# Optimization experiments

Hardware: AMD Instinct MI355X
Metric: run time of the kernel (lower is better)

## Reference

```python
import jax, jax.numpy as jnp
import numpy as np
import math

S = 8192
D = 128

def setup_inputs() -> dict:
    key = jax.random.key(0)
    kq, kk, kv = jax.random.split(key, 3)
    q = jax.random.normal(kq, (S, D), dtype=jnp.float32)
    k = jax.random.normal(kk, (S, D), dtype=jnp.float32)
    v = jax.random.normal(kv, (S, D), dtype=jnp.float32)
    return {"q": q, "k": k, "v": v}

def reference(q, k, v):
    # scores: [Sq, Sk], scaled by sqrt(head_dim)
    scale = 1.0 / math.sqrt(q.shape[1])
    scores = jnp.einsum('qd,kd->qk', q, k) * scale
    # causal mask: tril kept, strict upper triangle -> -inf (mask=True)
    causal = jnp.tril(jnp.ones((q.shape[0], k.shape[0]), dtype=bool))
    scores = jnp.where(causal, scores, -jnp.inf)
    # softmax over keys (dim=1), numerically stable
    attn = jax.nn.softmax(scores, axis=1)
    return jnp.einsum('qk,kd->qd', attn, v)
```

## Files before the change

kernel.cpp:

```cpp
#include <hip/hip_runtime.h>

#define S_TOTAL 8192
#define D_DIM   128
#define QBLK    256
#define NQT     32
#define NSPL    16
#define UNITS   512
#define TILEB   16384
#define QSCALE  0.12751879523178264f
#define NEG_BIG -1.0e30f
#define THR     8.0f

typedef __attribute__((ext_vector_type(8)))  short    bf16x8;
typedef __attribute__((ext_vector_type(16))) float    f32x16;
typedef __attribute__((ext_vector_type(4)))  float    f32x4;
typedef __attribute__((ext_vector_type(4)))  unsigned u32x4;

static __device__ __forceinline__ unsigned short f2bf(float f) {
    unsigned int u = __builtin_bit_cast(unsigned int, f);
    u += 0x7FFFu + ((u >> 16) & 1u);
    return (unsigned short)(u >> 16);
}
static __device__ __forceinline__ float bf2f(unsigned short u) {
    return __builtin_bit_cast(float, (unsigned int)u << 16);
}
static __device__ __forceinline__ void glds16(const void* g, void* l) {
    __builtin_amdgcn_global_load_lds(
        (const __attribute__((address_space(1))) void*)g,
        (__attribute__((address_space(3))) void*)l, 16, 0, 0);
}
static __device__ __forceinline__ unsigned pk2(float lo, float hi) {
    unsigned r;
    asm("v_cvt_pk_bf16_f32 %0, %1, %2" : "=v"(r) : "v"(lo), "v"(hi));
    return r;
}
static __device__ __forceinline__ void pl32swap(unsigned& x, unsigned& y) {
    asm("v_permlane32_swap_b32 %0, %1" : "+v"(x), "+v"(y));
}

__global__ __launch_bounds__(256)
void prep_q(const float* __restrict__ Q, unsigned short* __restrict__ Qbf)
{
    int i4 = blockIdx.x * 256 + threadIdx.x;
    const float4 v = reinterpret_cast<const float4*>(Q)[i4];
    ushort4 o;
    o.x = f2bf(v.x * QSCALE); o.y = f2bf(v.y * QSCALE);
    o.z = f2bf(v.z * QSCALE); o.w = f2bf(v.w * QSCALE);
    reinterpret_cast<ushort4*>(Qbf)[i4] = o;
}

__global__ __launch_bounds__(256)
void prep_k(const float* __restrict__ K, unsigned short* __restrict__ Kswz)
{
    int c = blockIdx.x * 256 + threadIdx.x;
    int t = c >> 10;
    int r = (c >> 4) & 63;
    int slot = c & 15;
    int d0 = (slot ^ (r & 15)) << 3;
    const float* src = K + ((size_t)t * 64 + r) * D_DIM + d0;
    float4 a = *reinterpret_cast<const float4*>(src);
    float4 b = *reinterpret_cast<const float4*>(src + 4);
    bf16x8 o;
    o[0] = (short)f2bf(a.x); o[1] = (short)f2bf(a.y);
    o[2] = (short)f2bf(a.z); o[3] = (short)f2bf(a.w);
    o[4] = (short)f2bf(b.x); o[5] = (short)f2bf(b.y);
    o[6] = (short)f2bf(b.z); o[7] = (short)f2bf(b.w);
    *reinterpret_cast<bf16x8*>(&Kswz[(size_t)c * 8]) = o;
}

__global__ __launch_bounds__(256)
void prep_v(const float* __restrict__ V, unsigned short* __restrict__ Vt)
{
    __shared__ float sv[64 * 68];
    int t = blockIdx.x >> 1;
    int h = blockIdx.x & 1;
    #pragma unroll
    for (int it = 0; it < 4; ++it) {
        int f4 = it * 256 + threadIdx.x;
        int r   = f4 >> 4;
        int c16 = (f4 & 15) << 2;
        float4 v = *reinterpret_cast<const float4*>(
            V + ((size_t)t * 64 + r) * D_DIM + h * 64 + c16);
        sv[r * 68 + c16 + 0] = v.x;
        sv[r * 68 + c16 + 1] = v.y;
        sv[r * 68 + c16 + 2] = v.z;
        sv[r * 68 + c16 + 3] = v.w;
    }
    __syncthreads();
    #pragma unroll
    for (int ii = 0; ii < 2; ++ii) {
        int cl = threadIdx.x * 2 + ii;
        int dl = cl >> 3;
        int slot = cl & 7;
        int d = h * 64 + dl;
        int k0 = (slot ^ (d & 7)) << 3;
        bf16x8 o;
        #pragma unroll
        for (int i = 0; i < 8; ++i) o[i] = (short)f2bf(sv[(k0 + i) * 68 + dl]);
        *reinterpret_cast<bf16x8*>(&Vt[(size_t)t * 8192 + ((size_t)(d * 8 + slot)) * 8]) = o;
    }
}

#define PROC_SUB(QF, ACC, MR, LR, QSB)                                        \
  {                                                                           \
    const int qg_ = (QSB) + qc;                                               \
    f32x16 sc;                                                                \
    _Pragma("unroll")                                                         \
    for (int r = 0; r < 16; ++r) sc[r] = 0.0f;                                \
    {                                                                         \
      const int rK_ = kj * 32 + qc;                                           \
      __builtin_amdgcn_s_setprio(1);                                          \
      _Pragma("unroll")                                                       \
      for (int dc = 0; dc < 8; ++dc) {                                        \
        int slot_ = ((dc << 1) | hi) ^ (rK_ & 15);                            \
        bf16x8 kf_ = *reinterpret_cast<const bf16x8*>(                        \
            bK + (rK_ << 8) + (slot_ << 4));                                  \
        sc = __builtin_amdgcn_mfma_f32_32x32x16_bf16(kf_, QF[dc], sc, 0, 0, 0); \
      }                                                                       \
      __builtin_amdgcn_s_setprio(0);                                          \
    }                                                                         \
    if (kbase + 31 > (QSB)) {                                                 \
      _Pragma("unroll")                                                       \
      for (int r = 0; r < 16; ++r) {                                          \
        int kg_ = kbase + (r & 3) + 8 * (r >> 2) + 4 * hi;                    \
        if (kg_ > qg_) sc[r] = -INFINITY;                                     \
      }                                                                       \
    }                                                                         \
    float ma_ = fmaxf(fmaxf(sc[0],  sc[1]),  fmaxf(sc[2],  sc[3]));           \
    float mb_ = fmaxf(fmaxf(sc[4],  sc[5]),  fmaxf(sc[6],  sc[7]));           \
    float mc_ = fmaxf(fmaxf(sc[8],  sc[9]),  fmaxf(sc[10], sc[11]));          \
    float md_ = fmaxf(fmaxf(sc[12], sc[13]), fmaxf(sc[14], sc[15]));          \
    float mx_ = fmaxf(fmaxf(ma_, mb_), fmaxf(mc_, md_));                      \
    float tmax_ = fmaxf(mx_, __shfl_xor(mx_, 32));                            \
    if (__any(tmax_ > MR + THR)) {                                            \
      float mn_ = fmaxf(MR, tmax_);                                           \
      float fs_ = __builtin_amdgcn_exp2f(MR - mn_);                           \
      MR = mn_;                                                               \
      LR *= fs_;                                                              \
      _Pragma("unroll")                                                       \
      for (int dt = 0; dt < 4; ++dt)                                          \
        _Pragma("unroll")                                                     \
        for (int r = 0; r < 16; ++r) ACC[dt][r] *= fs_;                       \
    }                                                                         \
    float s0_ = 0.f, s1_ = 0.f, s2_ = 0.f, s3_ = 0.f;                         \
    _Pragma("unroll")                                                         \
    for (int r = 0; r < 16; r += 4) {                                         \
      float p0_ = __builtin_amdgcn_exp2f(sc[r + 0] - MR);                     \
      float p1_ = __builtin_amdgcn_exp2f(sc[r + 1] - MR);                     \
      float p2_ = __builtin_amdgcn_exp2f(sc[r + 2] - MR);                     \
      float p3_ = __builtin_amdgcn_exp2f(sc[r + 3] - MR);                     \
      sc[r + 0] = p0_; sc[r + 1] = p1_; sc[r + 2] = p2_; sc[r + 3] = p3_;     \
      s0_ += p0_; s1_ += p1_; s2_ += p2_; s3_ += p3_;                         \
    }                                                                         \
    float lt_ = (s0_ + s1_) + (s2_ + s3_);                                    \
    lt_ += __shfl_xor(lt_, 32);                                               \
    LR += lt_;                                                                \
    _Pragma("unroll")                                                         \
    for (int cl = 0; cl < 2; ++cl) {                                          \
      const int rb_ = cl * 8;                                                 \
      const int ck_ = kj * 2 + cl;                                            \
      unsigned pa_ = pk2(sc[rb_ + 0], sc[rb_ + 1]);                           \
      unsigned pb_ = pk2(sc[rb_ + 4], sc[rb_ + 5]);                           \
      unsigned pc_ = pk2(sc[rb_ + 2], sc[rb_ + 3]);                           \
      unsigned pd_ = pk2(sc[rb_ + 6], sc[rb_ + 7]);                           \
      pl32swap(pa_, pb_);                                                     \
      pl32swap(pc_, pd_);                                                     \
      u32x4 t4_ = {pa_, pc_, pb_, pd_};                                       \
      bf16x8 pf_ = __builtin_bit_cast(bf16x8, t4_);                           \
      __builtin_amdgcn_s_setprio(1);                                          \
      _Pragma("unroll")                                                       \
      for (int dt = 0; dt < 4; ++dt) {                                        \
        int dV_ = dt * 32 + qc;                                               \
        int slot_ = ((ck_ << 1) | hi) ^ (dV_ & 7);                            \
        bf16x8 vf_ = *reinterpret_cast<const bf16x8*>(                        \
            bV + (dV_ << 7) + (slot_ << 4));                                  \
        ACC[dt] = __builtin_amdgcn_mfma_f32_32x32x16_bf16(vf_, pf_, ACC[dt], 0, 0, 0); \
      }                                                                       \
      __builtin_amdgcn_s_setprio(0);                                          \
    }                                                                         \
  }

#define EPI_SUB(ACC, ROFF, MR, LR)                                            \
  {                                                                           \
    _Pragma("unroll")                                                         \
    for (int dt = 0; dt < 4; ++dt)                                            \
      _Pragma("unroll")                                                       \
      for (int i = 0; i < 8; ++i) {                                           \
        unsigned pk_ = pk2(ACC[dt][2 * i], ACC[dt][2 * i + 1]);               \
        int d_ = dt * 32 + (i & 1) * 2 + (i >> 1) * 8 + 4 * hi;               \
        *reinterpret_cast<unsigned*>(&sOw[qc * 136 + d_]) = pk_;              \
      }                                                                       \
    _Pragma("unroll")                                                         \
    for (int it = 0; it < 8; ++it) {                                          \
      int flat_ = it * 64 + lane;                                             \
      int q_  = flat_ >> 4;                                                   \
      int s8_ = flat_ & 15;                                                   \
      bf16x8 v_ = *reinterpret_cast<const bf16x8*>(&sOw[q_ * 136 + s8_ * 8]); \
      __builtin_nontemporal_store(v_, reinterpret_cast<bf16x8*>(              \
          OB + ((size_t)(w * 64 + (ROFF) + q_)) * D_DIM + s8_ * 8));          \
    }                                                                         \
    if (hi == 0) {                                                            \
      mpart[unit * QBLK + w * 64 + (ROFF) + qc] = MR;                         \
      lpart[unit * QBLK + w * 64 + (ROFF) + qc] = LR;                         \
    }                                                                         \
  }

__global__ __launch_bounds__(256, 2)
void attn16(const unsigned short* __restrict__ Qbf,
            const unsigned short* __restrict__ Kswz,
            const unsigned short* __restrict__ Vtswz,
            unsigned short* __restrict__ Opart,
            float* __restrict__ mpart, float* __restrict__ lpart)
{
    __shared__ char sbuf[2][2 * TILEB];

    const int bx = (int)blockIdx.x;
    const int p  = bx >> 4;
    const int s  = bx & 15;
    const int qt = (p < 16) ? (31 - p) : (p - 16);
    const int unit   = qt * NSPL + s;
    const int jtiles = 4 * qt + 4;

    const int tid  = threadIdx.x;
    const int w    = tid >> 6;
    const int lane = tid & 63;
    const int qc   = lane & 31;
    const int hi   = lane >> 5;

    const int qw0 = qt * QBLK + w * 64;

    bf16x8 qf0[8], qf1[8];
    #pragma unroll
    for (int dc = 0; dc < 8; ++dc) {
        qf0[dc] = *reinterpret_cast<const bf16x8*>(
            Qbf + (size_t)(qw0 + qc) * D_DIM + dc * 16 + hi * 8);
        qf1[dc] = *reinterpret_cast<const bf16x8*>(
            Qbf + (size_t)(qw0 + 32 + qc) * D_DIM + dc * 16 + hi * 8);
    }

    f32x16 acc0[4], acc1[4];
    #pragma unroll
    for (int dt = 0; dt < 4; ++dt)
        #pragma unroll
        for (int r = 0; r < 16; ++r) { acc0[dt][r] = 0.0f; acc1[dt][r] = 0.0f; }
    float m0r = NEG_BIG, l0r = 0.0f, m1r = NEG_BIG, l1r = 0.0f;

    auto STAGE = [&](int c, int j) {
        const char* gK = (const char*)Kswz + (size_t)j * TILEB;
        const char* gV = (const char*)Vtswz + (size_t)j * TILEB;
        char* lK = sbuf[c];
        char* lV = sbuf[c] + TILEB;
        #pragma unroll
        for (int it = 0; it < 4; ++it) {
            int goff = (it * 256 + tid) * 16;
            int loff = (it * 256 + (w << 6)) * 16;
            glds16(gK + goff, lK + loff);
            glds16(gV + goff, lV + loff);
        }
    };

    int j = s, c = 0;
    if (j < jtiles) {
        STAGE(0, j);
        __syncthreads();
        for (; j < jtiles; j += NSPL) {
            int jn = j + NSPL;
            if (jn < jtiles) STAGE(c ^ 1, jn);

            const char* bK = sbuf[c];
            const char* bV = sbuf[c] + TILEB;

            #pragma unroll
            for (int kj = 0; kj < 2; ++kj) {
                const int kbase = j * 64 + kj * 32;
                if (kbase <= qw0 + 63) {
                    if (kbase <= qw0 + 31)
                        PROC_SUB(qf0, acc0, m0r, l0r, qw0);
                    PROC_SUB(qf1, acc1, m1r, l1r, qw0 + 32);
                }
            }
            __syncthreads();
            c ^= 1;
        }
    }

    unsigned short* OB = Opart + (size_t)unit * (QBLK * D_DIM);
    unsigned short* sOw = reinterpret_cast<unsigned short*>(&sbuf[0][0])
                          + w * (32 * 136 + 16);
    EPI_SUB(acc0, 0,  m0r, l0r);
    EPI_SUB(acc1, 32, m1r, l1r);
}

__global__ __launch_bounds__(256)
void attn_mergeF(const unsigned short* __restrict__ Opart,
                 const float* __restrict__ mpart, const float* __restrict__ lpart,
                 float* __restrict__ Og)
{
    int tid = threadIdx.x;
    int row = blockIdx.x * 16 + (tid >> 4);
    int c8  = tid & 15;
    int qt    = row >> 8;
    int local = row & 255;
    int base  = qt * NSPL;

    float M = NEG_BIG;
    for (int s = 0; s < NSPL; ++s)
        M = fmaxf(M, mpart[(size_t)(base + s) * QBLK + local]);
    float L = 0.0f;
    for (int s = 0; s < NSPL; ++s)
        L += __builtin_amdgcn_exp2f(mpart[(size_t)(base + s) * QBLK + local] - M)
             * lpart[(size_t)(base + s) * QBLK + local];
    float invL = 1.0f / L;

    float a[8] = {0.f, 0.f, 0.f, 0.f, 0.f, 0.f, 0.f, 0.f};
    for (int s = 0; s < NSPL; ++s) {
        float e = __builtin_amdgcn_exp2f(mpart[(size_t)(base + s) * QBLK + local] - M);
        bf16x8 o = __builtin_nontemporal_load(reinterpret_cast<const bf16x8*>(
            &Opart[((size_t)(base + s) * QBLK + local) * D_DIM + c8 * 8]));
        #pragma unroll
        for (int i = 0; i < 8; ++i)
            a[i] += e * bf2f((unsigned short)o[i]);
    }
    float4 w0 = {a[0] * invL, a[1] * invL, a[2] * invL, a[3] * invL};
    float4 w1 = {a[4] * invL, a[5] * invL, a[6] * invL, a[7] * invL};
    float* dst = Og + (size_t)row * D_DIM + c8 * 8;
    *reinterpret_cast<float4*>(dst)     = w0;
    *reinterpret_cast<float4*>(dst + 4) = w1;
}

__global__ __launch_bounds__(256, 2)
void attn_f32(const float* __restrict__ Qg, const float* __restrict__ Kg,
              const float* __restrict__ Vg, float* __restrict__ Og)
{
    __shared__ unsigned short sK [64 * 128];
    __shared__ unsigned short sVt[128 * 64];
    __shared__ unsigned short sP [4 * 16 * 72];

    const int qt   = (int)gridDim.y - 1 - (int)blockIdx.y;
    const int tid  = threadIdx.x;
    const int w    = tid >> 6;
    const int lane = tid & 63;
    const int g    = lane >> 4;
    const int lr   = lane & 15;

    const int qrow_base  = qt * 64 + w * 16 + g * 4;
    const int q_frag_row = qt * 64 + w * 16 + lr;

    bf16x8 qa[4];
    #pragma unroll
    for (int dc = 0; dc < 4; ++dc) {
        const float* src = Qg + q_frag_row * D_DIM + dc * 32 + g * 8;
        bf16x8 v;
        #pragma unroll
        for (int i = 0; i < 8; ++i) v[i] = (short)f2bf(src[i]);
        qa[dc] = v;
    }

    f32x4 acc[8];
    #pragma unroll
    for (int dj = 0; dj < 8; ++dj) acc[dj] = f32x4{0.f, 0.f, 0.f, 0.f};
    float m_run[4], l_run[4];
    #pragma unroll
    for (int r = 0; r < 4; ++r) { m_run[r] = -INFINITY; l_run[r] = 0.0f; }

    const float scale = 0.08838834764831845f;
    const int jtiles = qt + 1;
    unsigned short* sPw = sP + w * (16 * 72);
    char* sKc = reinterpret_cast<char*>(sK);
    char* sVc = reinterpret_cast<char*>(sVt);

    for (int j = 0; j < jtiles; ++j) {
        __syncthreads();
        #pragma unroll
        for (int it = 0; it < 8; ++it) {
            int flat4 = it * 256 + tid;
            int r  = flat4 >> 5;
            int d0 = (flat4 & 31) << 2;
            const float4 kv = *reinterpret_cast<const float4*>(
                Kg + (j * 64 + r) * D_DIM + d0);
            ushort4 wv;
            wv.x = f2bf(kv.x); wv.y = f2bf(kv.y); wv.z = f2bf(kv.z); wv.w = f2bf(kv.w);
            int byte = (r << 8) | (((d0 >> 3) ^ (r & 15)) << 4) | ((d0 & 7) << 1);
            *reinterpret_cast<ushort4*>(sKc + byte) = wv;
        }
        {
            int d = tid & 127;
            int khalf = tid >> 7;
            #pragma unroll
            for (int it = 0; it < 8; ++it) {
                int k0 = it * 8 + khalf * 4;
                const float* vsrc = Vg + (j * 64 + k0) * D_DIM + d;
                ushort4 wv;
                wv.x = f2bf(vsrc[0 * D_DIM]); wv.y = f2bf(vsrc[1 * D_DIM]);
                wv.z = f2bf(vsrc[2 * D_DIM]); wv.w = f2bf(vsrc[3 * D_DIM]);
                int byte = (d << 7) | (((k0 >> 3) ^ (d & 7)) << 4) | ((k0 & 7) << 1);
                *reinterpret_cast<ushort4*>(sVc + byte) = wv;
            }
        }
        __syncthreads();

        f32x4 sf[4];
        #pragma unroll
        for (int kj = 0; kj < 4; ++kj) {
            f32x4 accs = f32x4{0.f, 0.f, 0.f, 0.f};
            #pragma unroll
            for (int dc = 0; dc < 4; ++dc) {
                int rowk = kj * 16 + lr;
                int slot = (dc * 4 + g) ^ lr;
                bf16x8 b = *reinterpret_cast<bf16x8*>(sKc + ((rowk << 8) | (slot << 4)));
                accs = __builtin_amdgcn_mfma_f32_16x16x32_bf16(qa[dc], b, accs, 0, 0, 0);
            }
            sf[kj] = accs;
        }
        #pragma unroll
        for (int kj = 0; kj < 4; ++kj)
            #pragma unroll
            for (int r = 0; r < 4; ++r)
                sf[kj][r] *= scale;
        if (j == qt) {
            #pragma unroll
            for (int kj = 0; kj < 4; ++kj) {
                int kglob = j * 64 + kj * 16 + lr;
                #pragma unroll
                for (int r = 0; r < 4; ++r)
                    if (kglob > qrow_base + r) sf[kj][r] = -INFINITY;
            }
        }
        float tmax[4];
        #pragma unroll
        for (int r = 0; r < 4; ++r)
            tmax[r] = fmaxf(fmaxf(sf[0][r], sf[1][r]), fmaxf(sf[2][r], sf[3][r]));
        #pragma unroll
        for (int off = 1; off < 16; off <<= 1)
            #pragma unroll
            for (int r = 0; r < 4; ++r)
                tmax[r] = fmaxf(tmax[r], __shfl_xor(tmax[r], off));
        float fsc[4], lt[4];
        #pragma unroll
        for (int r = 0; r < 4; ++r) {
            float mn = fmaxf(m_run[r], tmax[r]);
            fsc[r] = __expf(m_run[r] - mn);
            m_run[r] = mn;
            lt[r] = 0.0f;
        }
        #pragma unroll
        for (int kj = 0; kj < 4; ++kj)
            #pragma unroll
            for (int r = 0; r < 4; ++r) {
                float p = __expf(sf[kj][r] - m_run[r]);
                sf[kj][r] = p;
                lt[r] += p;
            }
        #pragma unroll
        for (int off = 1; off < 16; off <<= 1)
            #pragma unroll
            for (int r = 0; r < 4; ++r)
                lt[r] += __shfl_xor(lt[r], off);
        #pragma unroll
        for (int r = 0; r < 4; ++r)
            l_run[r] = l_run[r] * fsc[r] + lt[r];
        #pragma unroll
        for (int dj = 0; dj < 8; ++dj)
            #pragma unroll
            for (int r = 0; r < 4; ++r)
                acc[dj][r] *= fsc[r];
        #pragma unroll
        for (int kj = 0; kj < 4; ++kj)
            #pragma unroll
            for (int r = 0; r < 4; ++r)
                sPw[(g * 4 + r) * 72 + kj * 16 + lr] = f2bf(sf[kj][r]);
        bf16x8 pa[2];
        #pragma unroll
        for (int kc = 0; kc < 2; ++kc)
            pa[kc] = *reinterpret_cast<bf16x8*>(sPw + lr * 72 + kc * 32 + g * 8);
        #pragma unroll
        for (int dj = 0; dj < 8; ++dj) {
            #pragma unroll
            for (int kc = 0; kc < 2; ++kc) {
                int d = dj * 16 + lr;
                int slot = (kc * 4 + g) ^ (lr & 7);
                bf16x8 b = *reinterpret_cast<bf16x8*>(sVc + ((d << 7) | (slot << 4)));
                acc[dj] = __builtin_amdgcn_mfma_f32_16x16x32_bf16(pa[kc], b, acc[dj], 0, 0, 0);
            }
        }
    }
    #pragma unroll
    for (int r = 0; r < 4; ++r) {
        float inv = 1.0f / l_run[r];
        int row = qrow_base + r;
        #pragma unroll
        for (int dj = 0; dj < 8; ++dj)
            Og[row * D_DIM + dj * 16 + lr] = acc[dj][r] * inv;
    }
}

extern "C" void kernel_launch(void* const* d_in, const int* in_sizes, int n_in,
                              void* d_out, int out_size, void* d_ws, size_t ws_size,
                              hipStream_t stream)
{
    const float* Qg = (const float*)d_in[0];
    const float* Kg = (const float*)d_in[1];
    const float* Vg = (const float*)d_in[2];
    float* Og = (float*)d_out;

    const size_t bfElems = (size_t)S_TOTAL * D_DIM;
    const size_t need = 3 * bfElems * 2
                      + (size_t)UNITS * ((size_t)QBLK * D_DIM * 2
                                         + (size_t)QBLK * 8);

    if (d_ws == nullptr || ws_size < need) {
        hipLaunchKernelGGL(attn_f32, dim3(1, 128), dim3(256), 0, stream,
                           Qg, Kg, Vg, Og);
        return;
    }

    unsigned short* Qbf   = (unsigned short*)d_ws;
    unsigned short* Kswz  = Qbf + bfElems;
    unsigned short* Vt    = Kswz + bfElems;
    unsigned short* Opart = Vt + bfElems;
    float* mpart = (float*)(Opart + (size_t)UNITS * QBLK * D_DIM);
    float* lpart = mpart + (size_t)UNITS * QBLK;

    hipLaunchKernelGGL(prep_q, dim3(1024), dim3(256), 0, stream, Qg, Qbf);
    hipLaunchKernelGGL(prep_k, dim3(512),  dim3(256), 0, stream, Kg, Kswz);
    hipLaunchKernelGGL(prep_v, dim3(256),  dim3(256), 0, stream, Vg, Vt);

    hipLaunchKernelGGL(attn16, dim3(UNITS), dim3(256), 0, stream,
                       Qbf, Kswz, Vt, Opart, mpart, lpart);
    hipLaunchKernelGGL(attn_mergeF, dim3(S_TOTAL / 16), dim3(256), 0, stream,
                       Opart, mpart, lpart, Og);
}
```

Baseline: 69.03 us.

## Fuse Q conversion into attention, merge K/V prep, interleave two sub-tiles

Drops the separate prep_q kernel and instead loads fp32 Q in the attention kernel, converting and scaling it in registers. prep_k and prep_v are merged into one launch selected by block index, cutting kernel launches from five to three. The per-subtile processing is split into QK^T, softmax and PV macros, and the two query sub-tiles are interleaved so one sub-tile's MFMA work can overlap the other's softmax. The causal mask is now applied unconditionally and the qf0 sub-tile skip for fully masked key blocks is removed, which adds redundant work on diagonal tiles and raises register pressure.

After: 84.13 us. 1.22x slower.

```diff
diff --git a/kernel.cpp b/kernel.cpp
--- a/kernel.cpp
+++ b/kernel.cpp
@@ -39,97 +39,83 @@
 }
 
 __global__ __launch_bounds__(256)
-void prep_q(const float* __restrict__ Q, unsigned short* __restrict__ Qbf)
-{
-    int i4 = blockIdx.x * 256 + threadIdx.x;
-    const float4 v = reinterpret_cast<const float4*>(Q)[i4];
-    ushort4 o;
-    o.x = f2bf(v.x * QSCALE); o.y = f2bf(v.y * QSCALE);
-    o.z = f2bf(v.z * QSCALE); o.w = f2bf(v.w * QSCALE);
-    reinterpret_cast<ushort4*>(Qbf)[i4] = o;
-}
-
-__global__ __launch_bounds__(256)
-void prep_k(const float* __restrict__ K, unsigned short* __restrict__ Kswz)
-{
-    int c = blockIdx.x * 256 + threadIdx.x;
-    int t = c >> 10;
-    int r = (c >> 4) & 63;
-    int slot = c & 15;
-    int d0 = (slot ^ (r & 15)) << 3;
-    const float* src = K + ((size_t)t * 64 + r) * D_DIM + d0;
-    float4 a = *reinterpret_cast<const float4*>(src);
-    float4 b = *reinterpret_cast<const float4*>(src + 4);
-    bf16x8 o;
-    o[0] = (short)f2bf(a.x); o[1] = (short)f2bf(a.y);
-    o[2] = (short)f2bf(a.z); o[3] = (short)f2bf(a.w);
-    o[4] = (short)f2bf(b.x); o[5] = (short)f2bf(b.y);
-    o[6] = (short)f2bf(b.z); o[7] = (short)f2bf(b.w);
-    *reinterpret_cast<bf16x8*>(&Kswz[(size_t)c * 8]) = o;
-}
-
-__global__ __launch_bounds__(256)
-void prep_v(const float* __restrict__ V, unsigned short* __restrict__ Vt)
+void prep_kv(const float* __restrict__ K, const float* __restrict__ V,
+             unsigned short* __restrict__ Kswz, unsigned short* __restrict__ Vt)
 {
     __shared__ float sv[64 * 68];
-    int t = blockIdx.x >> 1;
-    int h = blockIdx.x & 1;
-    #pragma unroll
-    for (int it = 0; it < 4; ++it) {
-        int f4 = it * 256 + threadIdx.x;
-        int r   = f4 >> 4;
-        int c16 = (f4 & 15) << 2;
-        float4 v = *reinterpret_cast<const float4*>(
-            V + ((size_t)t * 64 + r) * D_DIM + h * 64 + c16);
-        sv[r * 68 + c16 + 0] = v.x;
-        sv[r * 68 + c16 + 1] = v.y;
-        sv[r * 68 + c16 + 2] = v.z;
-        sv[r * 68 + c16 + 3] = v.w;
-    }
-    __syncthreads();
-    #pragma unroll
-    for (int ii = 0; ii < 2; ++ii) {
-        int cl = threadIdx.x * 2 + ii;
-        int dl = cl >> 3;
-        int slot = cl & 7;
-        int d = h * 64 + dl;
-        int k0 = (slot ^ (d & 7)) << 3;
+    const int b   = (int)blockIdx.x;
+    const int tid = threadIdx.x;
+
+    if (b < 512) {
+        int c = b * 256 + tid;
+        int t = c >> 10;
+        int r = (c >> 4) & 63;
+        int slot = c & 15;
+        int d0 = (slot ^ (r & 15)) << 3;
+        const float* src = K + ((size_t)t * 64 + r) * D_DIM + d0;
+        float4 a  = *reinterpret_cast<const float4*>(src);
+        float4 bq = *reinterpret_cast<const float4*>(src + 4);
         bf16x8 o;
-        #pragma unroll
-        for (int i = 0; i < 8; ++i) o[i] = (short)f2bf(sv[(k0 + i) * 68 + dl]);
-        *reinterpret_cast<bf16x8*>(&Vt[(size_t)t * 8192 + ((size_t)(d * 8 + slot)) * 8]) = o;
-    }
-}
-
-#define PROC_SUB(QF, ACC, MR, LR, QSB)                                        \
-  {                                                                           \
-    const int qg_ = (QSB) + qc;                                               \
-    f32x16 sc;                                                                \
+        o[0] = (short)f2bf(a.x);  o[1] = (short)f2bf(a.y);
+        o[2] = (short)f2bf(a.z);  o[3] = (short)f2bf(a.w);
+        o[4] = (short)f2bf(bq.x); o[5] = (short)f2bf(bq.y);
+        o[6] = (short)f2bf(bq.z); o[7] = (short)f2bf(bq.w);
+        *reinterpret_cast<bf16x8*>(&Kswz[(size_t)c * 8]) = o;
+    } else {
+        int bb = b - 512;
+        int t = bb >> 1;
+        int h = bb & 1;
+        #pragma unroll
+        for (int it = 0; it < 4; ++it) {
+            int f4 = it * 256 + tid;
+            int r   = f4 >> 4;
+            int c16 = (f4 & 15) << 2;
+            float4 v = *reinterpret_cast<const float4*>(
+                V + ((size_t)t * 64 + r) * D_DIM + h * 64 + c16);
+            sv[r * 68 + c16 + 0] = v.x;
+            sv[r * 68 + c16 + 1] = v.y;
+            sv[r * 68 + c16 + 2] = v.z;
+            sv[r * 68 + c16 + 3] = v.w;
+        }
+        __syncthreads();
+        #pragma unroll
+        for (int ii = 0; ii < 2; ++ii) {
+            int cl = tid * 2 + ii;
+            int dl = cl >> 3;
+            int slot = cl & 7;
+            int d = h * 64 + dl;
+            int k0 = (slot ^ (d & 7)) << 3;
+            bf16x8 o;
+            #pragma unroll
+            for (int i = 0; i < 8; ++i) o[i] = (short)f2bf(sv[(k0 + i) * 68 + dl]);
+            *reinterpret_cast<bf16x8*>(&Vt[(size_t)t * 8192 + ((size_t)(d * 8 + slot)) * 8]) = o;
+        }
+    }
+}
+
+#define QKT_M(SC, QF)                                                         \
+  { _Pragma("unroll")                                                         \
+    for (int r = 0; r < 16; ++r) SC[r] = 0.0f;                                \
+    __builtin_amdgcn_s_setprio(1);                                            \
     _Pragma("unroll")                                                         \
-    for (int r = 0; r < 16; ++r) sc[r] = 0.0f;                                \
-    {                                                                         \
-      const int rK_ = kj * 32 + qc;                                           \
-      __builtin_amdgcn_s_setprio(1);                                          \
-      _Pragma("unroll")                                                       \
-      for (int dc = 0; dc < 8; ++dc) {                                        \
-        int slot_ = ((dc << 1) | hi) ^ (rK_ & 15);                            \
-        bf16x8 kf_ = *reinterpret_cast<const bf16x8*>(                        \
-            bK + (rK_ << 8) + (slot_ << 4));                                  \
-        sc = __builtin_amdgcn_mfma_f32_32x32x16_bf16(kf_, QF[dc], sc, 0, 0, 0); \
-      }                                                                       \
-      __builtin_amdgcn_s_setprio(0);                                          \
+    for (int dc = 0; dc < 8; ++dc) {                                          \
+      bf16x8 kf_ = *reinterpret_cast<const bf16x8*>(                          \
+          bK + (rK << 8) + ((((dc << 1) | hi) ^ (rK & 15)) << 4));            \
+      SC = __builtin_amdgcn_mfma_f32_32x32x16_bf16(kf_, QF[dc], SC, 0, 0, 0); \
     }                                                                         \
-    if (kbase + 31 > (QSB)) {                                                 \
-      _Pragma("unroll")                                                       \
-      for (int r = 0; r < 16; ++r) {                                          \
-        int kg_ = kbase + (r & 3) + 8 * (r >> 2) + 4 * hi;                    \
-        if (kg_ > qg_) sc[r] = -INFINITY;                                     \
-      }                                                                       \
+    __builtin_amdgcn_s_setprio(0); }
+
+#define SM_M(SC, MR, LR, ACC, QSB)                                            \
+  { const int qg_ = (QSB) + qc;                                               \
+    _Pragma("unroll")                                                         \
+    for (int r = 0; r < 16; ++r) {                                            \
+      int kg_ = kbase + (r & 3) + 8 * (r >> 2) + 4 * hi;                      \
+      SC[r] = (kg_ > qg_) ? -INFINITY : SC[r];                                \
     }                                                                         \
-    float ma_ = fmaxf(fmaxf(sc[0],  sc[1]),  fmaxf(sc[2],  sc[3]));           \
-    float mb_ = fmaxf(fmaxf(sc[4],  sc[5]),  fmaxf(sc[6],  sc[7]));           \
-    float mc_ = fmaxf(fmaxf(sc[8],  sc[9]),  fmaxf(sc[10], sc[11]));          \
-    float md_ = fmaxf(fmaxf(sc[12], sc[13]), fmaxf(sc[14], sc[15]));          \
+    float ma_ = fmaxf(fmaxf(SC[0],  SC[1]),  fmaxf(SC[2],  SC[3]));           \
+    float mb_ = fmaxf(fmaxf(SC[4],  SC[5]),  fmaxf(SC[6],  SC[7]));           \
+    float mc_ = fmaxf(fmaxf(SC[8],  SC[9]),  fmaxf(SC[10], SC[11]));          \
+    float md_ = fmaxf(fmaxf(SC[12], SC[13]), fmaxf(SC[14], SC[15]));          \
     float mx_ = fmaxf(fmaxf(ma_, mb_), fmaxf(mc_, md_));                      \
     float tmax_ = fmaxf(mx_, __shfl_xor(mx_, 32));                            \
     if (__any(tmax_ > MR + THR)) {                                            \
@@ -145,24 +131,26 @@
     float s0_ = 0.f, s1_ = 0.f, s2_ = 0.f, s3_ = 0.f;                         \
     _Pragma("unroll")                                                         \
     for (int r = 0; r < 16; r += 4) {                                         \
-      float p0_ = __builtin_amdgcn_exp2f(sc[r + 0] - MR);                     \
-      float p1_ = __builtin_amdgcn_exp2f(sc[r + 1] - MR);                     \
-      float p2_ = __builtin_amdgcn_exp2f(sc[r + 2] - MR);                     \
-      float p3_ = __builtin_amdgcn_exp2f(sc[r + 3] - MR);                     \
-      sc[r + 0] = p0_; sc[r + 1] = p1_; sc[r + 2] = p2_; sc[r + 3] = p3_;     \
+      float p0_ = __builtin_amdgcn_exp2f(SC[r + 0] - MR);                     \
+      float p1_ = __builtin_amdgcn_exp2f(SC[r + 1] - MR);                     \
+      float p2_ = __builtin_amdgcn_exp2f(SC[r + 2] - MR);                     \
+      float p3_ = __builtin_amdgcn_exp2f(SC[r + 3] - MR);                     \
+      SC[r + 0] = p0_; SC[r + 1] = p1_; SC[r + 2] = p2_; SC[r + 3] = p3_;     \
       s0_ += p0_; s1_ += p1_; s2_ += p2_; s3_ += p3_;                         \
     }                                                                         \
     float lt_ = (s0_ + s1_) + (s2_ + s3_);                                    \
     lt_ += __shfl_xor(lt_, 32);                                               \
-    LR += lt_;                                                                \
-    _Pragma("unroll")                                                         \
+    LR += lt_; }
+
+#define PV_M(SC, ACC)                                                         \
+  { _Pragma("unroll")                                                         \
     for (int cl = 0; cl < 2; ++cl) {                                          \
       const int rb_ = cl * 8;                                                 \
       const int ck_ = kj * 2 + cl;                                            \
-      unsigned pa_ = pk2(sc[rb_ + 0], sc[rb_ + 1]);                           \
-      unsigned pb_ = pk2(sc[rb_ + 4], sc[rb_ + 5]);                           \
-      unsigned pc_ = pk2(sc[rb_ + 2], sc[rb_ + 3]);                           \
-      unsigned pd_ = pk2(sc[rb_ + 6], sc[rb_ + 7]);                           \
+      unsigned pa_ = pk2(SC[rb_ + 0], SC[rb_ + 1]);                           \
+      unsigned pb_ = pk2(SC[rb_ + 4], SC[rb_ + 5]);                           \
+      unsigned pc_ = pk2(SC[rb_ + 2], SC[rb_ + 3]);                           \
+      unsigned pd_ = pk2(SC[rb_ + 6], SC[rb_ + 7]);                           \
       pl32swap(pa_, pb_);                                                     \
       pl32swap(pc_, pd_);                                                     \
       u32x4 t4_ = {pa_, pc_, pb_, pd_};                                       \
@@ -177,8 +165,7 @@
         ACC[dt] = __builtin_amdgcn_mfma_f32_32x32x16_bf16(vf_, pf_, ACC[dt], 0, 0, 0); \
       }                                                                       \
       __builtin_amdgcn_s_setprio(0);                                          \
-    }                                                                         \
-  }
+    } }
 
 #define EPI_SUB(ACC, ROFF, MR, LR)                                            \
   {                                                                           \
@@ -206,11 +193,11 @@
   }
 
 __global__ __launch_bounds__(256, 2)
-void attn16(const unsigned short* __restrict__ Qbf,
-            const unsigned short* __restrict__ Kswz,
-            const unsigned short* __restrict__ Vtswz,
-            unsigned short* __restrict__ Opart,
-            float* __restrict__ mpart, float* __restrict__ lpart)
+void attn16b(const float* __restrict__ Qg,
+             const unsigned short* __restrict__ Kswz,
+             const unsigned short* __restrict__ Vtswz,
+             unsigned short* __restrict__ Opart,
+             float* __restrict__ mpart, float* __restrict__ lpart)
 {
     __shared__ char sbuf[2][2 * TILEB];
 
@@ -232,10 +219,23 @@
     bf16x8 qf0[8], qf1[8];
     #pragma unroll
     for (int dc = 0; dc < 8; ++dc) {
-        qf0[dc] = *reinterpret_cast<const bf16x8*>(
-            Qbf + (size_t)(qw0 + qc) * D_DIM + dc * 16 + hi * 8);
-        qf1[dc] = *reinterpret_cast<const bf16x8*>(
-            Qbf + (size_t)(qw0 + 32 + qc) * D_DIM + dc * 16 + hi * 8);
+        const float* s0 = Qg + (size_t)(qw0 + qc) * D_DIM + dc * 16 + hi * 8;
+        const float* s1 = Qg + (size_t)(qw0 + 32 + qc) * D_DIM + dc * 16 + hi * 8;
+        float4 a0 = *reinterpret_cast<const float4*>(s0);
+        float4 b0 = *reinterpret_cast<const float4*>(s0 + 4);
+        float4 a1 = *reinterpret_cast<const float4*>(s1);
+        float4 b1 = *reinterpret_cast<const float4*>(s1 + 4);
+        bf16x8 v0, v1;
+        v0[0] = (short)f2bf(a0.x * QSCALE); v0[1] = (short)f2bf(a0.y * QSCALE);
+        v0[2] = (short)f2bf(a0.z * QSCALE); v0[3] = (short)f2bf(a0.w * QSCALE);
+        v0[4] = (short)f2bf(b0.x * QSCALE); v0[5] = (short)f2bf(b0.y * QSCALE);
+        v0[6] = (short)f2bf(b0.z * QSCALE); v0[7] = (short)f2bf(b0.w * QSCALE);
+        v1[0] = (short)f2bf(a1.x * QSCALE); v1[1] = (short)f2bf(a1.y * QSCALE);
+        v1[2] = (short)f2bf(a1.z * QSCALE); v1[3] = (short)f2bf(a1.w * QSCALE);
+        v1[4] = (short)f2bf(b1.x * QSCALE); v1[5] = (short)f2bf(b1.y * QSCALE);
+        v1[6] = (short)f2bf(b1.z * QSCALE); v1[7] = (short)f2bf(b1.w * QSCALE);
+        qf0[dc] = v0;
+        qf1[dc] = v1;
     }
 
     f32x16 acc0[4], acc1[4];
@@ -274,9 +274,14 @@
             for (int kj = 0; kj < 2; ++kj) {
                 const int kbase = j * 64 + kj * 32;
                 if (kbase <= qw0 + 63) {
-                    if (kbase <= qw0 + 31)
-                        PROC_SUB(qf0, acc0, m0r, l0r, qw0);
-                    PROC_SUB(qf1, acc1, m1r, l1r, qw0 + 32);
+                    const int rK = kj * 32 + qc;
+                    f32x16 sc0, sc1;
+                    QKT_M(sc0, qf0);
+                    SM_M(sc0, m0r, l0r, acc0, qw0);
+                    QKT_M(sc1, qf1);
+                    PV_M(sc0, acc0);
+                    SM_M(sc1, m1r, l1r, acc1, qw0 + 32);
+                    PV_M(sc1, acc1);
                 }
             }
             __syncthreads();
@@ -504,7 +509,7 @@
     float* Og = (float*)d_out;
 
     const size_t bfElems = (size_t)S_TOTAL * D_DIM;
-    const size_t need = 3 * bfElems * 2
+    const size_t need = 2 * bfElems * 2
                       + (size_t)UNITS * ((size_t)QBLK * D_DIM * 2
                                          + (size_t)QBLK * 8);
 
@@ -514,19 +519,16 @@
         return;
     }
 
-    unsigned short* Qbf   = (unsigned short*)d_ws;
-    unsigned short* Kswz  = Qbf + bfElems;
+    unsigned short* Kswz  = (unsigned short*)d_ws;
     unsigned short* Vt    = Kswz + bfElems;
     unsigned short* Opart = Vt + bfElems;
     float* mpart = (float*)(Opart + (size_t)UNITS * QBLK * D_DIM);
     float* lpart = mpart + (size_t)UNITS * QBLK;
 
-    hipLaunchKernelGGL(prep_q, dim3(1024), dim3(256), 0, stream, Qg, Qbf);
-    hipLaunchKernelGGL(prep_k, dim3(512),  dim3(256), 0, stream, Kg, Kswz);
-    hipLaunchKernelGGL(prep_v, dim3(256),  dim3(256), 0, stream, Vg, Vt);
-
-    hipLaunchKernelGGL(attn16, dim3(UNITS), dim3(256), 0, stream,
-                       Qbf, Kswz, Vt, Opart, mpart, lpart);
+    hipLaunchKernelGGL(prep_kv, dim3(768), dim3(256), 0, stream,
+                       Kg, Vg, Kswz, Vt);
+    hipLaunchKernelGGL(attn16b, dim3(UNITS), dim3(256), 0, stream,
+                       Qg, Kswz, Vt, Opart, mpart, lpart);
     hipLaunchKernelGGL(attn_mergeF, dim3(S_TOTAL / 16), dim3(256), 0, stream,
                        Opart, mpart, lpart, Og);
 }
```
